# Performance work log

Hardware: AMD Instinct MI355X
Metric: run time of the kernel (lower is better)

## Reference

```python
import jax, jax.numpy as jnp
import numpy as np

N = 50000
E = 800000
H = 96
NUM_IN = 11
PE_DIM = 24
NUM_OUT = 1
NUM_LAYERS = 4
NUM_GRAPHS = 256


def _linear_params(key, d_in, d_out):
    k1, k2 = jax.random.split(key)
    bound = 1.0 / np.sqrt(d_in)
    w = jax.random.uniform(k1, (d_in, d_out), jnp.float32, -bound, bound)
    b = jax.random.uniform(k2, (d_out,), jnp.float32, -bound, bound)
    return w, b


def setup_inputs() -> dict:
    key = jax.random.key(0)
    ks = jax.random.split(key, 32)
    x = jax.random.normal(ks[0], (N, NUM_IN), jnp.float32)
    pos = jax.random.normal(ks[1], (N, 3), jnp.float32)
    pe = jax.random.normal(ks[2], (N, PE_DIM), jnp.float32)
    edge_index = jax.random.randint(ks[3], (2, E), 0, N, jnp.int64)
    batch = jnp.sort(jax.random.randint(ks[4], (N,), 0, NUM_GRAPHS, jnp.int64))
    embed_w1, embed_b1 = _linear_params(ks[5], NUM_IN + PE_DIM, H)
    embed_w2, embed_b2 = _linear_params(ks[6], H, H)
    # per-layer stacked params
    msg_w1 = []; msg_b1 = []; msg_w2 = []; msg_b2 = []
    upd_w1 = []; upd_b1 = []; upd_w2 = []; upd_b2 = []
    for l in range(NUM_LAYERS):
        w, b = _linear_params(ks[7 + l], 2 * H + 1, H); msg_w1.append(w); msg_b1.append(b)
        w, b = _linear_params(ks[11 + l], H, H); msg_w2.append(w); msg_b2.append(b)
        w, b = _linear_params(ks[15 + l], 2 * H, H); upd_w1.append(w); upd_b1.append(b)
        w, b = _linear_params(ks[19 + l], H, H); upd_w2.append(w); upd_b2.append(b)
    pre_w1, pre_b1 = _linear_params(ks[23], H, H)
    pre_w2, pre_b2 = _linear_params(ks[24], H, H)
    ro_w1, ro_b1 = _linear_params(ks[25], H, H)
    ro_w2, ro_b2 = _linear_params(ks[26], H, NUM_OUT)
    return {
        'x': x, 'pos': pos, 'pe': pe, 'edge_index': edge_index, 'batch': batch,
        'embed_w1': embed_w1, 'embed_b1': embed_b1, 'embed_w2': embed_w2, 'embed_b2': embed_b2,
        'msg_w1': jnp.stack(msg_w1), 'msg_b1': jnp.stack(msg_b1),
        'msg_w2': jnp.stack(msg_w2), 'msg_b2': jnp.stack(msg_b2),
        'upd_w1': jnp.stack(upd_w1), 'upd_b1': jnp.stack(upd_b1),
        'upd_w2': jnp.stack(upd_w2), 'upd_b2': jnp.stack(upd_b2),
        'pre_w1': pre_w1, 'pre_b1': pre_b1, 'pre_w2': pre_w2, 'pre_b2': pre_b2,
        'ro_w1': ro_w1, 'ro_b1': ro_b1, 'ro_w2': ro_w2, 'ro_b2': ro_b2,
    }


def _egnn_forward(x, pos, pe, edge_index, batch,
                  embed_w1, embed_b1, embed_w2, embed_b2,
                  msg_w1, msg_b1, msg_w2, msg_b2,
                  upd_w1, upd_b1, upd_w2, upd_b2,
                  pre_w1, pre_b1, pre_w2, pre_b2,
                  ro_w1, ro_b1, ro_w2, ro_b2):
    silu = jax.nn.silu
    send, rec = edge_index[0], edge_index[1]
    h = jnp.concatenate([x, pe], axis=-1)
    h = silu(h @ embed_w1 + embed_b1) @ embed_w2 + embed_b2  # [N,H]
    dist = jnp.linalg.norm(pos[send] - pos[rec], axis=1)[:, None]  # [E,1]
    for l in range(NUM_LAYERS):
        state = jnp.concatenate([h[send], h[rec], dist], axis=1)  # [E,2H+1]
        msg = silu(silu(state @ msg_w1[l] + msg_b1[l]) @ msg_w2[l] + msg_b2[l])  # [E,H]
        aggr = jax.ops.segment_sum(msg, rec, num_segments=h.shape[0])  # [N,H]
        upd_in = jnp.concatenate([h, aggr], axis=1)
        update = silu(upd_in @ upd_w1[l] + upd_b1[l]) @ upd_w2[l] + upd_b2[l]
        h = h + update
    h = silu(h @ pre_w1 + pre_b1) @ pre_w2 + pre_b2
    pooled = jax.ops.segment_sum(h, batch, num_segments=NUM_GRAPHS)  # [G,H]
    out = silu(pooled @ ro_w1 + ro_b1) @ ro_w2 + ro_b2  # [G,1]
    return jnp.squeeze(out)


def reference(x, pos, pe, edge_index, batch,
              embed_w1, embed_b1, embed_w2, embed_b2,
              msg_w1, msg_b1, msg_w2, msg_b2,
              upd_w1, upd_b1, upd_w2, upd_b2,
              pre_w1, pre_b1, pre_w2, pre_b2,
              ro_w1, ro_b1, ro_w2, ro_b2):
    return _egnn_forward(x, pos, pe, edge_index, batch,
                         embed_w1, embed_b1, embed_w2, embed_b2,
                         msg_w1, msg_b1, msg_w2, msg_b2,
                         upd_w1, upd_b1, upd_w2, upd_b2,
                         pre_w1, pre_b1, pre_w2, pre_b2,
                         ro_w1, ro_b1, ro_w2, ro_b2)
```

## Files before the change

### kernel.cpp

```cpp
#include <hip/hip_runtime.h>
#include <hip/hip_bf16.h>

#define HDIM 96
#define TILE 128

typedef __attribute__((ext_vector_type(8))) short  short8;
typedef __attribute__((ext_vector_type(4))) short  short4v;
typedef __attribute__((ext_vector_type(4))) float  float4v;
typedef __attribute__((ext_vector_type(4))) unsigned int uint4v;

static __device__ __forceinline__ short f2bf(float f){
    __hip_bfloat16 h = __float2bfloat16(f);
    return *reinterpret_cast<short*>(&h);
}
static __device__ __forceinline__ float bf2f(short s){
    unsigned u = ((unsigned)(unsigned short)s) << 16;
    return __uint_as_float(u);
}
static __device__ __forceinline__ float silu_f(float v){
    return v * __builtin_amdgcn_rcpf(1.0f + __expf(-v));
}

struct SwJob { const float* src; int ck; int ks; int ksrc; };
struct SwTable { SwJob j[22]; };

__global__ __launch_bounds__(256) void swizzle_kernel(SwTable T, short* __restrict__ dst, int total){
    int gid = blockIdx.x*256 + threadIdx.x;
    if (gid >= total) return;
    int ksg = gid / 3072;
    int e   = gid % 3072;
    const float* src = T.j[0].src; int k0 = 0, ksrc = 0;
    #pragma unroll
    for (int jj = 0; jj < 22; ++jj){
        int s = T.j[jj].ck;
        if (ksg >= s && ksg < s + T.j[jj].ks){ src = T.j[jj].src; k0 = (ksg - s)*32; ksrc = T.j[jj].ksrc; }
    }
    int nt   = e >> 9;
    int rem  = e & 511;
    int lane = rem >> 3;
    int jx   = rem & 7;
    int k = k0 + ((lane >> 4) << 3) + jx;
    int f = nt*16 + (lane & 15);
    float v = (k < ksrc) ? src[(size_t)k*HDIM + f] : 0.0f;
    dst[gid] = f2bf(v);
}

__global__ __launch_bounds__(256) void swizzle2_kernel(const float* __restrict__ msg_w1,
                                                       short* __restrict__ dst, int total){
    int gid = blockIdx.x*256 + threadIdx.x;
    if (gid >= total) return;
    int layer = gid / 18432;
    int e     = gid % 18432;
    int ksg = e / 6144;
    int rem = e % 6144;
    int nt   = rem >> 9;
    int r2   = rem & 511;
    int lane = r2 >> 3;
    int jx   = r2 & 7;
    int k = ksg*32 + ((lane >> 4) << 3) + jx;
    int f = nt*16 + (lane & 15);
    int row = (f < 96) ? k : (96 + k);
    int col = (f < 96) ? f : (f - 96);
    dst[gid] = f2bf(msg_w1[(size_t)layer*193*96 + (size_t)row*96 + col]);
}

__global__ __launch_bounds__(256) void hist_kernel(const int* __restrict__ rec, int* __restrict__ deg, int E){
    int e = blockIdx.x*256 + threadIdx.x;
    if (e < E) atomicAdd(&deg[rec[e]], 1);
}

__global__ __launch_bounds__(256) void scan_part(const int* __restrict__ deg, int* __restrict__ part, int N){
    __shared__ int red[256];
    const int t = threadIdx.x;
    int base = blockIdx.x*1024;
    int s = 0;
    #pragma unroll
    for (int j=0;j<4;j++){ int i = base + j*256 + t; s += (i<N)?deg[i]:0; }
    red[t]=s; __syncthreads();
    #pragma unroll
    for (int off=128; off>0; off>>=1){ if (t<off) red[t]+=red[t+off]; __syncthreads(); }
    if (t==0) part[blockIdx.x]=red[0];
}
__global__ __launch_bounds__(256) void scan_top(int* __restrict__ part, int nb){
    __shared__ int buf[256];
    const int t = threadIdx.x;
    int v = (t < nb) ? part[t] : 0;
    buf[t] = v;
    __syncthreads();
    #pragma unroll
    for (int off=1; off<256; off<<=1){
        int u = (t>=off)?buf[t-off]:0;
        __syncthreads();
        buf[t] += u;
        __syncthreads();
    }
    if (t < nb) part[t] = buf[t] - v;
}
__global__ __launch_bounds__(256) void scan_final(const int* __restrict__ deg, const int* __restrict__ part,
                                                  int* __restrict__ cur, int N){
    __shared__ int tsum[256];
    const int t = threadIdx.x;
    int i0 = blockIdx.x*1024 + t*4;
    int a0 = (i0+0<N)?deg[i0+0]:0;
    int a1 = (i0+1<N)?deg[i0+1]:0;
    int a2 = (i0+2<N)?deg[i0+2]:0;
    int a3 = (i0+3<N)?deg[i0+3]:0;
    int s = a0+a1+a2+a3;
    tsum[t]=s; __syncthreads();
    #pragma unroll
    for (int off=1; off<256; off<<=1){
        int u = (t>=off)?tsum[t-off]:0;
        __syncthreads();
        tsum[t]+=u;
        __syncthreads();
    }
    int excl = tsum[t]-s + part[blockIdx.x];
    if (i0+0<N) cur[i0+0]=excl;
    if (i0+1<N) cur[i0+1]=excl+a0;
    if (i0+2<N) cur[i0+2]=excl+a0+a1;
    if (i0+3<N) cur[i0+3]=excl+a0+a1+a2;
}

__global__ __launch_bounds__(256) void scatter_kernel(
    const int* __restrict__ send, const int* __restrict__ rec, const float* __restrict__ pos,
    int* __restrict__ cur, int* __restrict__ send_s, int* __restrict__ rec_s,
    float* __restrict__ dist_s, int E)
{
    int e = blockIdx.x*256 + threadIdx.x;
    if (e >= E) return;
    int s = send[e], r = rec[e];
    int p = atomicAdd(&cur[r], 1);
    send_s[p] = s;
    rec_s[p]  = r;
    float dx = pos[3*s]   - pos[3*r];
    float dy = pos[3*s+1] - pos[3*r+1];
    float dz = pos[3*s+2] - pos[3*r+2];
    dist_s[p] = sqrtf(dx*dx + dy*dy + dz*dz);
}

__global__ __launch_bounds__(256,5) void edge_kernel(
    const short* __restrict__ SR,
    const int* __restrict__ send_s, const int* __restrict__ rec_s, const float* __restrict__ dist_s,
    const float* __restrict__ w1r192,
    const short* __restrict__ w2sw, const float* __restrict__ b2,
    float* __restrict__ aggr, int E)
{
    __shared__ short msgS[TILE*104];
    __shared__ int   recS[TILE];
    __shared__ int   startIdxS[TILE+1];
    __shared__ int   wcntS[2];
    const int t  = threadIdx.x;
    const int e0 = blockIdx.x * TILE;

    if (t < TILE) {
        int e = e0 + t; if (e >= E) e = E - 1;
        recS[t] = rec_s[e];
    }
    __syncthreads();

    bool flag = false;
    if (t < TILE) flag = (t == 0) || (recS[t] != recS[t-1]);
    unsigned long long bmask = __ballot(flag ? 1 : 0);
    int pre = __popcll(bmask & ((1ull << (t & 63)) - 1ull));
    if (t < TILE && (t & 63) == 0) wcntS[t >> 6] = __popcll(bmask);
    __syncthreads();
    const int nseg = wcntS[0] + wcntS[1];
    if (flag) startIdxS[pre + ((t >> 6) ? wcntS[0] : 0)] = t;
    if (t == 0) startIdxS[nseg] = TILE;

    const bool firstB = (e0 > 0) && (rec_s[e0-1] == recS[0]);
    const bool lastB  = (e0 + TILE < E) && (rec_s[e0 + TILE] == recS[TILE-1]);

    const int lane = t & 63;
    const int wv   = t >> 6;
    const int e_lo = wv * 32;
    const int col  = lane & 15;
    const int quad = lane >> 4;
    const int frow = quad * 4;
    const float4v fzero = {0.f,0.f,0.f,0.f};

    short8 frag[2][3];
    #pragma unroll
    for (int et=0; et<2; ++et){
        int ei = e_lo + et*16 + col;
        int ec = e0 + ei; if (ec >= E) ec = E - 1;
        int se = send_s[ec];
        int re = recS[ei];
        float d = dist_s[ec];
        #pragma unroll
        for (int ks=0; ks<3; ++ks){
            int f0 = ks*32 + quad*8;
            short8 S8 = *(const short8*)(SR + (size_t)se*192 + f0);
            short8 R8 = *(const short8*)(SR + (size_t)re*192 + 96 + f0);
            float4v wa = *(const float4v*)(w1r192 + f0);
            float4v wb = *(const float4v*)(w1r192 + f0 + 4);
            short8 fr;
            #pragma unroll
            for (int j=0;j<8;j++){
                float w = (j<4) ? wa[j] : wb[j-4];
                float v = bf2f(S8[j]) + bf2f(R8[j]) + d*w;
                fr[j] = f2bf(silu_f(v));
            }
            frag[et][ks] = fr;
        }
    }

    float4v acc2[2][6];
    #pragma unroll
    for (int i=0;i<2;i++)
      #pragma unroll
      for (int n=0;n<6;n++) acc2[i][n] = fzero;

    const short8* w2f = (const short8*)w2sw;
    #pragma unroll
    for (int ks = 0; ks < 3; ++ks) {
        #pragma unroll
        for (int mt = 0; mt < 6; ++mt) {
            short8 a = w2f[(ks*6+mt)*64 + lane];
            acc2[0][mt] = __builtin_amdgcn_mfma_f32_16x16x32_bf16(a, frag[0][ks], acc2[0][mt], 0, 0, 0);
            acc2[1][mt] = __builtin_amdgcn_mfma_f32_16x16x32_bf16(a, frag[1][ks], acc2[1][mt], 0, 0, 0);
        }
    }
    float4v b2v[6];
    #pragma unroll
    for (int mt=0; mt<6; ++mt) b2v[mt] = *(const float4v*)(b2 + mt*16 + frow);

    #pragma unroll
    for (int et=0; et<2; ++et){
        int e = e_lo + et*16 + col;
        bool valid = (e0 + e) < E;
        #pragma unroll
        for (int mt=0; mt<6; ++mt){
            short4v sv;
            #pragma unroll
            for (int r=0;r<4;r++){
                float u = silu_f(acc2[et][mt][r] + b2v[mt][r]);
                sv[r] = f2bf(valid ? u : 0.0f);
            }
            *(short4v*)(msgS + e*104 + mt*16 + frow) = sv;
        }
    }
    __syncthreads();

    const int items = nseg * 12;
    for (int item = t; item < items; item += 256){
        int s  = item / 12;
        int fg = item - s*12;
        int r0 = startIdxS[s], r1 = startIdxS[s+1];
        float sum[8] = {0.f,0.f,0.f,0.f,0.f,0.f,0.f,0.f};
        for (int r = r0; r < r1; ++r){
            short8 v8 = *(const short8*)(msgS + r*104 + fg*8);
            #pragma unroll
            for (int j=0;j<8;j++) sum[j] += bf2f(v8[j]);
        }
        float* dstp = aggr + (size_t)recS[r0]*HDIM + fg*8;
        bool bnd = (s == 0 && firstB) || (s == nseg-1 && lastB);
        if (bnd) {
            #pragma unroll
            for (int j=0;j<8;j++) atomicAdd(dstp+j, sum[j]);
        } else {
            float4v lo = {sum[0], sum[1], sum[2], sum[3]};
            float4v hi = {sum[4], sum[5], sum[6], sum[7]};
            *(float4v*)(dstp)     = lo;
            *(float4v*)(dstp + 4) = hi;
        }
    }
}

__global__ __launch_bounds__(256,3) void update_kernel(
    float* __restrict__ h, short* __restrict__ hbf, float* __restrict__ aggr,
    const short* __restrict__ w1sw, const float* __restrict__ b1,
    const short* __restrict__ w2sw, const float* __restrict__ b2,
    const short* __restrict__ w1sr_next, const float* __restrict__ msgb1_next,
    short* __restrict__ SR, int N)
{
    __shared__ short stateS[TILE*200];
    const int t  = threadIdx.x;
    const int n0 = blockIdx.x * TILE;

    #pragma unroll
    for (int it = 0; it < 12; ++it) {
        int q = it*256 + t;
        int c = q % 24;
        int i = q / 24;
        int node = n0 + i;
        if (c < 12) {
            uint4v v = {0u,0u,0u,0u};
            if (node < N) v = *(const uint4v*)(hbf + (size_t)node*HDIM + c*8);
            *(uint4v*)(stateS + i*200 + c*8) = v;
        } else {
            int cc = c - 12;
            short8 s8 = {0,0,0,0,0,0,0,0};
            if (node < N) {
                float4v a0 = *(const float4v*)(aggr + (size_t)node*HDIM + cc*8);
                float4v a1 = *(const float4v*)(aggr + (size_t)node*HDIM + cc*8 + 4);
                s8[0]=f2bf(a0[0]); s8[1]=f2bf(a0[1]); s8[2]=f2bf(a0[2]); s8[3]=f2bf(a0[3]);
                s8[4]=f2bf(a1[0]); s8[5]=f2bf(a1[1]); s8[6]=f2bf(a1[2]); s8[7]=f2bf(a1[3]);
            }
            *(short8*)(stateS + i*200 + HDIM + cc*8) = s8;
        }
    }
    __syncthreads();

    const int lane = t & 63;
    const int wv   = t >> 6;
    const int e_lo = wv * 32;
    const int col  = lane & 15;
    const int quad = lane >> 4;
    const int koff = quad * 8;
    const int frow = quad * 4;
    const float4v fzero = {0.f,0.f,0.f,0.f};

    float4v acc[2][6];
    #pragma unroll
    for (int i=0;i<2;i++)
      #pragma unroll
      for (int n=0;n<6;n++) acc[i][n] = fzero;

    const short8* w1f = (const short8*)w1sw;
    #pragma unroll
    for (int ks = 0; ks < 6; ++ks) {
        short8 bb0 = *(const short8*)(stateS + (e_lo+col)*200    + ks*32 + koff);
        short8 bb1 = *(const short8*)(stateS + (e_lo+16+col)*200 + ks*32 + koff);
        #pragma unroll
        for (int mt = 0; mt < 6; ++mt) {
            short8 a = w1f[(ks*6+mt)*64 + lane];
            acc[0][mt] = __builtin_amdgcn_mfma_f32_16x16x32_bf16(a, bb0, acc[0][mt], 0, 0, 0);
            acc[1][mt] = __builtin_amdgcn_mfma_f32_16x16x32_bf16(a, bb1, acc[1][mt], 0, 0, 0);
        }
    }
    float4v b1v[6];
    #pragma unroll
    for (int mt=0; mt<6; ++mt) b1v[mt] = *(const float4v*)(b1 + mt*16 + frow);
    __syncthreads();

    short* t1S = stateS;
    #pragma unroll
    for (int et=0; et<2; ++et){
        int e = e_lo + et*16 + col;
        #pragma unroll
        for (int mt=0; mt<6; ++mt){
            short4v sv;
            #pragma unroll
            for (int r=0;r<4;r++) sv[r] = f2bf(silu_f(acc[et][mt][r] + b1v[mt][r]));
            *(short4v*)(t1S + e*104 + mt*16 + frow) = sv;
        }
    }
    __syncthreads();

    float4v acc2[2][6];
    #pragma unroll
    for (int i=0;i<2;i++)
      #pragma unroll
      for (int n=0;n<6;n++) acc2[i][n] = fzero;

    const short8* w2f = (const short8*)w2sw;
    #pragma unroll
    for (int ks = 0; ks < 3; ++ks) {
        short8 bb0 = *(const short8*)(t1S + (e_lo+col)*104    + ks*32 + koff);
        short8 bb1 = *(const short8*)(t1S + (e_lo+16+col)*104 + ks*32 + koff);
        #pragma unroll
        for (int mt = 0; mt < 6; ++mt) {
            short8 a = w2f[(ks*6+mt)*64 + lane];
            acc2[0][mt] = __builtin_amdgcn_mfma_f32_16x16x32_bf16(a, bb0, acc2[0][mt], 0, 0, 0);
            acc2[1][mt] = __builtin_amdgcn_mfma_f32_16x16x32_bf16(a, bb1, acc2[1][mt], 0, 0, 0);
        }
    }
    float4v b2v[6];
    #pragma unroll
    for (int mt=0; mt<6; ++mt) b2v[mt] = *(const float4v*)(b2 + mt*16 + frow);
    __syncthreads();

    #pragma unroll
    for (int et=0; et<2; ++et){
        int erow = e_lo + et*16 + col;
        int node = n0 + erow;
        bool valid = node < N;
        size_t base = (size_t)node*HDIM;
        #pragma unroll
        for (int mt=0; mt<6; ++mt){
            int f0 = mt*16 + frow;
            float4v old = valid ? *(const float4v*)(h + base + f0) : fzero;
            float4v o;
            #pragma unroll
            for (int r=0;r<4;r++) o[r] = old[r] + acc2[et][mt][r] + b2v[mt][r];
            short4v sv = {f2bf(o[0]), f2bf(o[1]), f2bf(o[2]), f2bf(o[3])};
            if (valid) {
                *(float4v*)(h + base + f0) = o;
                *(short4v*)(hbf + base + f0) = sv;
                *(float4v*)(aggr + base + f0) = fzero;
            }
            *(short4v*)(stateS + erow*104 + f0) = sv;
        }
    }

    if (w1sr_next) {
        __syncthreads();
        float4v accS[2][12];
        #pragma unroll
        for (int i=0;i<2;i++)
          #pragma unroll
          for (int n=0;n<12;n++) accS[i][n] = fzero;

        const short8* wsf = (const short8*)w1sr_next;
        #pragma unroll
        for (int ks = 0; ks < 3; ++ks) {
            short8 bb0 = *(const short8*)(stateS + (e_lo+col)*104    + ks*32 + koff);
            short8 bb1 = *(const short8*)(stateS + (e_lo+16+col)*104 + ks*32 + koff);
            #pragma unroll
            for (int mt = 0; mt < 12; ++mt) {
                short8 a = wsf[(ks*12+mt)*64 + lane];
                accS[0][mt] = __builtin_amdgcn_mfma_f32_16x16x32_bf16(a, bb0, accS[0][mt], 0, 0, 0);
                accS[1][mt] = __builtin_amdgcn_mfma_f32_16x16x32_bf16(a, bb1, accS[1][mt], 0, 0, 0);
            }
        }
        float4v bnv[6];
        #pragma unroll
        for (int mt=0; mt<6; ++mt) bnv[mt] = *(const float4v*)(msgb1_next + mt*16 + frow);

        #pragma unroll
        for (int et=0; et<2; ++et){
            int node = n0 + e_lo + et*16 + col;
            if (node < N) {
                size_t sbase = (size_t)node*192;
                #pragma unroll
                for (int mt=0; mt<12; ++mt){
                    float4v o = accS[et][mt];
                    if (mt < 6) { o[0]+=bnv[mt][0]; o[1]+=bnv[mt][1]; o[2]+=bnv[mt][2]; o[3]+=bnv[mt][3]; }
                    short4v sv = {f2bf(o[0]), f2bf(o[1]), f2bf(o[2]), f2bf(o[3])};
                    *(short4v*)(SR + sbase + mt*16 + frow) = sv;
                }
            }
        }
    }
}

__global__ __launch_bounds__(256,3) void embed_kernel(
    const float* __restrict__ x, const float* __restrict__ pe,
    const short* __restrict__ w1sw, const float* __restrict__ b1,
    const short* __restrict__ w2sw, const float* __restrict__ b2,
    float* __restrict__ h, short* __restrict__ hbf,
    const short* __restrict__ w1sr0, const float* __restrict__ msgb1_0,
    short* __restrict__ SR, int N)
{
    __shared__ short stateS[TILE*72];
    __shared__ short t1S[TILE*104];
    const int t  = threadIdx.x;
    const int n0 = blockIdx.x * TILE;

    if (t < TILE) {
        int node = n0 + t;
        short* row = stateS + t*72;
        if (node < N) {
            #pragma unroll
            for (int j=0;j<11;j++) row[j]    = f2bf(x[(size_t)node*11 + j]);
            #pragma unroll
            for (int j=0;j<24;j++) row[11+j] = f2bf(pe[(size_t)node*24 + j]);
            #pragma unroll
            for (int j=35;j<64;j++) row[j] = 0;
        } else {
            #pragma unroll
            for (int j=0;j<64;j++) row[j] = 0;
        }
    }
    __syncthreads();

    const int lane = t & 63;
    const int wv   = t >> 6;
    const int e_lo = wv * 32;
    const int col  = lane & 15;
    const int quad = lane >> 4;
    const int koff = quad * 8;
    const int frow = quad * 4;
    const float4v fzero = {0.f,0.f,0.f,0.f};

    float4v acc[2][6];
    #pragma unroll
    for (int i=0;i<2;i++)
      #pragma unroll
      for (int n=0;n<6;n++) acc[i][n] = fzero;

    const short8* w1f = (const short8*)w1sw;
    #pragma unroll
    for (int ks = 0; ks < 2; ++ks) {
        short8 bb0 = *(const short8*)(stateS + (e_lo+col)*72    + ks*32 + koff);
        short8 bb1 = *(const short8*)(stateS + (e_lo+16+col)*72 + ks*32 + koff);
        #pragma unroll
        for (int mt = 0; mt < 6; ++mt) {
            short8 a = w1f[(ks*6+mt)*64 + lane];
            acc[0][mt] = __builtin_amdgcn_mfma_f32_16x16x32_bf16(a, bb0, acc[0][mt], 0, 0, 0);
            acc[1][mt] = __builtin_amdgcn_mfma_f32_16x16x32_bf16(a, bb1, acc[1][mt], 0, 0, 0);
        }
    }
    float4v b1v[6];
    #pragma unroll
    for (int mt=0; mt<6; ++mt) b1v[mt] = *(const float4v*)(b1 + mt*16 + frow);

    #pragma unroll
    for (int et=0; et<2; ++et){
        int e = e_lo + et*16 + col;
        #pragma unroll
        for (int mt=0; mt<6; ++mt){
            short4v sv;
            #pragma unroll
            for (int r=0;r<4;r++) sv[r] = f2bf(silu_f(acc[et][mt][r] + b1v[mt][r]));
            *(short4v*)(t1S + e*104 + mt*16 + frow) = sv;
        }
    }
    __syncthreads();

    float4v acc2[2][6];
    #pragma unroll
    for (int i=0;i<2;i++)
      #pragma unroll
      for (int n=0;n<6;n++) acc2[i][n] = fzero;

    const short8* w2f = (const short8*)w2sw;
    #pragma unroll
    for (int ks = 0; ks < 3; ++ks) {
        short8 bb0 = *(const short8*)(t1S + (e_lo+col)*104    + ks*32 + koff);
        short8 bb1 = *(const short8*)(t1S + (e_lo+16+col)*104 + ks*32 + koff);
        #pragma unroll
        for (int mt = 0; mt < 6; ++mt) {
            short8 a = w2f[(ks*6+mt)*64 + lane];
            acc2[0][mt] = __builtin_amdgcn_mfma_f32_16x16x32_bf16(a, bb0, acc2[0][mt], 0, 0, 0);
            acc2[1][mt] = __builtin_amdgcn_mfma_f32_16x16x32_bf16(a, bb1, acc2[1][mt], 0, 0, 0);
        }
    }
    float4v b2v[6];
    #pragma unroll
    for (int mt=0; mt<6; ++mt) b2v[mt] = *(const float4v*)(b2 + mt*16 + frow);
    __syncthreads();

    #pragma unroll
    for (int et=0; et<2; ++et){
        int erow = e_lo + et*16 + col;
        int node = n0 + erow;
        bool valid = node < N;
        size_t base = (size_t)node*HDIM;
        #pragma unroll
        for (int mt=0; mt<6; ++mt){
            int f0 = mt*16 + frow;
            float4v o;
            #pragma unroll
            for (int r=0;r<4;r++) o[r] = acc2[et][mt][r] + b2v[mt][r];
            short4v sv = {f2bf(o[0]), f2bf(o[1]), f2bf(o[2]), f2bf(o[3])};
            if (valid) {
                *(float4v*)(h + base + f0) = o;
                *(short4v*)(hbf + base + f0) = sv;
            }
            *(short4v*)(t1S + erow*104 + f0) = sv;
        }
    }
    __syncthreads();

    float4v accS[2][12];
    #pragma unroll
    for (int i=0;i<2;i++)
      #pragma unroll
      for (int n=0;n<12;n++) accS[i][n] = fzero;

    const short8* wsf = (const short8*)w1sr0;
    #pragma unroll
    for (int ks = 0; ks < 3; ++ks) {
        short8 bb0 = *(const short8*)(t1S + (e_lo+col)*104    + ks*32 + koff);
        short8 bb1 = *(const short8*)(t1S + (e_lo+16+col)*104 + ks*32 + koff);
        #pragma unroll
        for (int mt = 0; mt < 12; ++mt) {
            short8 a = wsf[(ks*12+mt)*64 + lane];
            accS[0][mt] = __builtin_amdgcn_mfma_f32_16x16x32_bf16(a, bb0, accS[0][mt], 0, 0, 0);
            accS[1][mt] = __builtin_amdgcn_mfma_f32_16x16x32_bf16(a, bb1, accS[1][mt], 0, 0, 0);
        }
    }
    float4v bnv[6];
    #pragma unroll
    for (int mt=0; mt<6; ++mt) bnv[mt] = *(const float4v*)(msgb1_0 + mt*16 + frow);

    #pragma unroll
    for (int et=0; et<2; ++et){
        int node = n0 + e_lo + et*16 + col;
        if (node < N) {
            size_t sbase = (size_t)node*192;
            #pragma unroll
            for (int mt=0; mt<12; ++mt){
                float4v o = accS[et][mt];
                if (mt < 6) { o[0]+=bnv[mt][0]; o[1]+=bnv[mt][1]; o[2]+=bnv[mt][2]; o[3]+=bnv[mt][3]; }
                short4v sv = {f2bf(o[0]), f2bf(o[1]), f2bf(o[2]), f2bf(o[3])};
                *(short4v*)(SR + sbase + mt*16 + frow) = sv;
            }
        }
    }
}

__global__ __launch_bounds__(256,2) void prepool_kernel(
    const short* __restrict__ hbf,
    const short* __restrict__ w1sw, const float* __restrict__ b1,
    const short* __restrict__ w2sw, const float* __restrict__ b2,
    const int* __restrict__ batch, float* __restrict__ pooled, int N)
{
    __shared__ short bufS[TILE*104*2];
    __shared__ int   batchS[TILE];
    __shared__ int   startIdxS[TILE+1];
    __shared__ int   wcntS[2];
    short* stateS = bufS;
    short* t1S    = bufS + TILE*104;
    float* msgS   = (float*)bufS;
    const int t  = threadIdx.x;
    const int n0 = blockIdx.x * TILE;

    #pragma unroll
    for (int it = 0; it < 6; ++it) {
        int q = it*256 + t;
        int c = q % 12;
        int i = q / 12;
        int node = n0 + i;
        uint4v v = {0u,0u,0u,0u};
        if (node < N) v = *(const uint4v*)(hbf + (size_t)node*HDIM + c*8);
        *(uint4v*)(stateS + i*104 + c*8) = v;
    }
    if (t < TILE) {
        int node = n0 + t;
        batchS[t] = batch[node < N ? node : N-1];
    }
    __syncthreads();

    bool flag = false;
    if (t < TILE) flag = (t == 0) || (batchS[t] != batchS[t-1]);
    unsigned long long bmask = __ballot(flag ? 1 : 0);
    int pre = __popcll(bmask & ((1ull << (t & 63)) - 1ull));
    if (t < TILE && (t & 63) == 0) wcntS[t >> 6] = __popcll(bmask);

    const int lane = t & 63;
    const int wv   = t >> 6;
    const int e_lo = wv * 32;
    const int col  = lane & 15;
    const int quad = lane >> 4;
    const int koff = quad * 8;
    const int frow = quad * 4;
    const float4v fzero = {0.f,0.f,0.f,0.f};

    float4v acc[2][6];
    #pragma unroll
    for (int i=0;i<2;i++)
      #pragma unroll
      for (int n=0;n<6;n++) acc[i][n] = fzero;

    const short8* w1f = (const short8*)w1sw;
    #pragma unroll
    for (int ks = 0; ks < 3; ++ks) {
        short8 bb0 = *(const short8*)(stateS + (e_lo+col)*104    + ks*32 + koff);
        short8 bb1 = *(const short8*)(stateS + (e_lo+16+col)*104 + ks*32 + koff);
        #pragma unroll
        for (int mt = 0; mt < 6; ++mt) {
            short8 a = w1f[(ks*6+mt)*64 + lane];
            acc[0][mt] = __builtin_amdgcn_mfma_f32_16x16x32_bf16(a, bb0, acc[0][mt], 0, 0, 0);
            acc[1][mt] = __builtin_amdgcn_mfma_f32_16x16x32_bf16(a, bb1, acc[1][mt], 0, 0, 0);
        }
    }
    float4v b1v[6];
    #pragma unroll
    for (int mt=0; mt<6; ++mt) b1v[mt] = *(const float4v*)(b1 + mt*16 + frow);

    #pragma unroll
    for (int et=0; et<2; ++et){
        int e = e_lo + et*16 + col;
        #pragma unroll
        for (int mt=0; mt<6; ++mt){
            short4v sv;
            #pragma unroll
            for (int r=0;r<4;r++) sv[r] = f2bf(silu_f(acc[et][mt][r] + b1v[mt][r]));
            *(short4v*)(t1S + e*104 + mt*16 + frow) = sv;
        }
    }
    __syncthreads();
    const int nseg = wcntS[0] + wcntS[1];
    if (flag) startIdxS[pre + ((t >> 6) ? wcntS[0] : 0)] = t;
    if (t == 0) startIdxS[nseg] = TILE;

    float4v acc2[2][6];
    #pragma unroll
    for (int i=0;i<2;i++)
      #pragma unroll
      for (int n=0;n<6;n++) acc2[i][n] = fzero;

    const short8* w2f = (const short8*)w2sw;
    #pragma unroll
    for (int ks = 0; ks < 3; ++ks) {
        short8 bb0 = *(const short8*)(t1S + (e_lo+col)*104    + ks*32 + koff);
        short8 bb1 = *(const short8*)(t1S + (e_lo+16+col)*104 + ks*32 + koff);
        #pragma unroll
        for (int mt = 0; mt < 6; ++mt) {
            short8 a = w2f[(ks*6+mt)*64 + lane];
            acc2[0][mt] = __builtin_amdgcn_mfma_f32_16x16x32_bf16(a, bb0, acc2[0][mt], 0, 0, 0);
            acc2[1][mt] = __builtin_amdgcn_mfma_f32_16x16x32_bf16(a, bb1, acc2[1][mt], 0, 0, 0);
        }
    }
    float4v b2v[6];
    #pragma unroll
    for (int mt=0; mt<6; ++mt) b2v[mt] = *(const float4v*)(b2 + mt*16 + frow);
    __syncthreads();

    #pragma unroll
    for (int et=0; et<2; ++et){
        int e = e_lo + et*16 + col;
        bool valid = (n0 + e) < N;
        #pragma unroll
        for (int mt=0; mt<6; ++mt){
            float4v v;
            #pragma unroll
            for (int r=0;r<4;r++){
                float u = acc2[et][mt][r] + b2v[mt][r];
                v[r] = valid ? u : 0.0f;
            }
            *(float4v*)(msgS + e*100 + mt*16 + frow) = v;
        }
    }
    __syncthreads();

    const int items = nseg * 24;
    for (int item = t; item < items; item += 256){
        int s  = item / 24;
        int fg = item - s*24;
        int r0 = startIdxS[s], r1 = startIdxS[s+1];
        float4v sum = fzero;
        for (int r = r0; r < r1; ++r) sum += *(const float4v*)(msgS + r*100 + fg*4);
        float* dstp = pooled + (size_t)batchS[r0]*HDIM + fg*4;
        atomicAdd(dstp+0, sum[0]);
        atomicAdd(dstp+1, sum[1]);
        atomicAdd(dstp+2, sum[2]);
        atomicAdd(dstp+3, sum[3]);
    }
}

__global__ __launch_bounds__(128) void readout_kernel(
    const float* __restrict__ pooled,
    const float* __restrict__ w1, const float* __restrict__ b1,
    const float* __restrict__ w2, const float* __restrict__ b2,
    float* __restrict__ out)
{
    __shared__ float red[128];
    const int g = blockIdx.x;
    const int t = threadIdx.x;
    float p = 0.0f;
    if (t < HDIM) {
        float acc = b1[t];
        for (int k = 0; k < HDIM; ++k)
            acc += pooled[(size_t)g*HDIM + k] * w1[(size_t)k*HDIM + t];
        acc = silu_f(acc);
        p = acc * w2[t];
    }
    red[t] = p;
    __syncthreads();
    for (int s = 64; s > 0; s >>= 1) {
        if (t < s) red[t] += red[t + s];
        __syncthreads();
    }
    if (t == 0) out[g] = red[0] + b2[0];
}

extern "C" void kernel_launch(void* const* d_in, const int* in_sizes, int n_in,
                              void* d_out, int out_size, void* d_ws, size_t ws_size,
                              hipStream_t stream)
{
    const float* x        = (const float*)d_in[0];
    const float* pos      = (const float*)d_in[1];
    const float* pe       = (const float*)d_in[2];
    const int*   ei       = (const int*)d_in[3];
    const int*   batch    = (const int*)d_in[4];
    const float* embed_w1 = (const float*)d_in[5];
    const float* embed_b1 = (const float*)d_in[6];
    const float* embed_w2 = (const float*)d_in[7];
    const float* embed_b2 = (const float*)d_in[8];
    const float* msg_w1   = (const float*)d_in[9];
    const float* msg_b1   = (const float*)d_in[10];
    const float* msg_w2   = (const float*)d_in[11];
    const float* msg_b2   = (const float*)d_in[12];
    const float* upd_w1   = (const float*)d_in[13];
    const float* upd_b1   = (const float*)d_in[14];
    const float* upd_w2   = (const float*)d_in[15];
    const float* upd_b2   = (const float*)d_in[16];
    const float* pre_w1   = (const float*)d_in[17];
    const float* pre_b1   = (const float*)d_in[18];
    const float* pre_w2   = (const float*)d_in[19];
    const float* pre_b2   = (const float*)d_in[20];
    const float* ro_w1    = (const float*)d_in[21];
    const float* ro_b1    = (const float*)d_in[22];
    const float* ro_w2    = (const float*)d_in[23];
    const float* ro_b2    = (const float*)d_in[24];

    const int E = in_sizes[3] / 2;
    const int N = in_sizes[4];
    const int G = out_size;

    char* ws = (char*)d_ws;
    size_t off = 0;
    auto alloc = [&](size_t bytes){ void* p = ws + off; off += (bytes + 255) & ~(size_t)255; return p; };
    float* h      = (float*)alloc((size_t)N*HDIM*4);
    short* hbf    = (short*)alloc((size_t)N*HDIM*2);
    float* aggr   = (float*)alloc((size_t)N*HDIM*4);
    float* pooled = (float*)alloc((size_t)G*HDIM*4);
    short* wsw    = (short*)alloc((size_t)59*3072*2);
    short* w1sr   = (short*)alloc((size_t)4*18432*2);
    short* SR     = (short*)alloc((size_t)N*192*2);
    int*   deg    = (int*)alloc((size_t)N*4);
    int*   cur    = (int*)alloc((size_t)N*4);
    int*   part   = (int*)alloc((size_t)256*4);
    int*   send_s = (int*)alloc((size_t)E*4);
    int*   rec_s  = (int*)alloc((size_t)E*4);
    float* dist_s = (float*)alloc((size_t)E*4);

    hipMemsetAsync(aggr,   0, (size_t)N*HDIM*4, stream);
    hipMemsetAsync(pooled, 0, (size_t)G*HDIM*4, stream);
    hipMemsetAsync(deg,    0, (size_t)N*4, stream);

    SwTable T;
    for (int jj=0;jj<22;jj++){ T.j[jj].src = embed_w1; T.j[jj].ck = 1<<30; T.j[jj].ks = 0; T.j[jj].ksrc = 0; }
    int ck = 0, ji = 0;
    auto add = [&](const float* s, int ks, int ksrc){
        T.j[ji].src = s; T.j[ji].ck = ck; T.j[ji].ks = ks; T.j[ji].ksrc = ksrc;
        ji++; ck += ks;
    };
    add(embed_w1, 2, 35);
    add(embed_w2, 3, 96);
    add(pre_w1,   3, 96);
    add(pre_w2,   3, 96);
    for (int l=0;l<4;l++) add(msg_w2 + (size_t)l*96*96,  3, 96);
    for (int l=0;l<4;l++) add(upd_w1 + (size_t)l*192*96, 6, 192);
    for (int l=0;l<4;l++) add(upd_w2 + (size_t)l*96*96,  3, 96);
    const int total = 59*3072;
    swizzle_kernel<<<(total+255)/256, 256, 0, stream>>>(T, wsw, total);
    const int total2 = 4*18432;
    swizzle2_kernel<<<(total2+255)/256, 256, 0, stream>>>(msg_w1, w1sr, total2);

    const int nbE256 = (E + 255) / 256;
    const int nbScan = (N + 1023) / 1024;
    hist_kernel<<<nbE256, 256, 0, stream>>>(ei + E, deg, E);
    scan_part<<<nbScan, 256, 0, stream>>>(deg, part, N);
    scan_top<<<1, 256, 0, stream>>>(part, nbScan);
    scan_final<<<nbScan, 256, 0, stream>>>(deg, part, cur, N);
    scatter_kernel<<<nbE256, 256, 0, stream>>>(ei, ei + E, pos, cur, send_s, rec_s, dist_s, E);

    const int nbN = (N + TILE - 1) / TILE;
    embed_kernel<<<nbN, 256, 0, stream>>>(x, pe, wsw + 0, embed_b1, wsw + 2*3072, embed_b2,
                                          h, hbf, w1sr, msg_b1, SR, N);

    const int nbE = (E + TILE - 1) / TILE;
    for (int l = 0; l < 4; ++l) {
        edge_kernel<<<nbE, 256, 0, stream>>>(SR, send_s, rec_s, dist_s,
            msg_w1 + (size_t)l*193*96 + (size_t)192*96,
            wsw + (11 + 3*l)*3072, msg_b2 + l*96, aggr, E);
        const short* w1sr_next = (l < 3) ? (w1sr + (size_t)(l+1)*18432) : nullptr;
        const float* msgb1_next = (l < 3) ? (msg_b1 + (l+1)*96) : nullptr;
        update_kernel<<<nbN, 256, 0, stream>>>(h, hbf, aggr,
            wsw + (23 + 6*l)*3072, upd_b1 + l*96,
            wsw + (47 + 3*l)*3072, upd_b2 + l*96,
            w1sr_next, msgb1_next, SR, N);
    }

    prepool_kernel<<<nbN, 256, 0, stream>>>(hbf, wsw + 5*3072, pre_b1, wsw + 8*3072, pre_b2,
                                            batch, pooled, N);
    readout_kernel<<<G, 128, 0, stream>>>(pooled, ro_w1, ro_b1, ro_w2, ro_b2, (float*)d_out);
}
```

Measured before the change: 766.1 us.

## Pack sender/dist into int2, shrink LDS stride, cheaper bf16 round, raise occupancy

Measured after the change: 879.3 us. 1.15x slower.

```diff
diff --git a/kernel.cpp b/kernel.cpp
--- a/kernel.cpp
+++ b/kernel.cpp
@@ -10,8 +10,8 @@
 typedef __attribute__((ext_vector_type(4))) unsigned int uint4v;
 
 static __device__ __forceinline__ short f2bf(float f){
-    __hip_bfloat16 h = __float2bfloat16(f);
-    return *reinterpret_cast<short*>(&h);
+    unsigned u = __float_as_uint(f);
+    return (short)((u + 0x8000u) >> 16);
 }
 static __device__ __forceinline__ float bf2f(short s){
     unsigned u = ((unsigned)(unsigned short)s) << 16;
@@ -123,29 +123,28 @@
 
 __global__ __launch_bounds__(256) void scatter_kernel(
     const int* __restrict__ send, const int* __restrict__ rec, const float* __restrict__ pos,
-    int* __restrict__ cur, int* __restrict__ send_s, int* __restrict__ rec_s,
-    float* __restrict__ dist_s, int E)
+    int* __restrict__ cur, int2* __restrict__ sd_s, int* __restrict__ rec_s, int E)
 {
     int e = blockIdx.x*256 + threadIdx.x;
     if (e >= E) return;
     int s = send[e], r = rec[e];
     int p = atomicAdd(&cur[r], 1);
-    send_s[p] = s;
-    rec_s[p]  = r;
     float dx = pos[3*s]   - pos[3*r];
     float dy = pos[3*s+1] - pos[3*r+1];
     float dz = pos[3*s+2] - pos[3*r+2];
-    dist_s[p] = sqrtf(dx*dx + dy*dy + dz*dz);
-}
-
-__global__ __launch_bounds__(256,5) void edge_kernel(
+    float d = sqrtf(dx*dx + dy*dy + dz*dz);
+    sd_s[p] = make_int2(s, __float_as_int(d));
+    rec_s[p] = r;
+}
+
+__global__ __launch_bounds__(256,6) void edge_kernel(
     const short* __restrict__ SR,
-    const int* __restrict__ send_s, const int* __restrict__ rec_s, const float* __restrict__ dist_s,
+    const int2* __restrict__ sd_s, const int* __restrict__ rec_s,
     const float* __restrict__ w1r192,
     const short* __restrict__ w2sw, const float* __restrict__ b2,
     float* __restrict__ aggr, int E)
 {
-    __shared__ short msgS[TILE*104];
+    __shared__ short msgS[TILE*100];
     __shared__ int   recS[TILE];
     __shared__ int   startIdxS[TILE+1];
     __shared__ int   wcntS[2];
@@ -184,9 +183,10 @@
     for (int et=0; et<2; ++et){
         int ei = e_lo + et*16 + col;
         int ec = e0 + ei; if (ec >= E) ec = E - 1;
-        int se = send_s[ec];
+        int2 sd = sd_s[ec];
+        int se = sd.x;
+        float d = __int_as_float(sd.y);
         int re = recS[ei];
-        float d = dist_s[ec];
         #pragma unroll
         for (int ks=0; ks<3; ++ks){
             int f0 = ks*32 + quad*8;
@@ -237,7 +237,7 @@
                 float u = silu_f(acc2[et][mt][r] + b2v[mt][r]);
                 sv[r] = f2bf(valid ? u : 0.0f);
             }
-            *(short4v*)(msgS + e*104 + mt*16 + frow) = sv;
+            *(short4v*)(msgS + e*100 + mt*16 + frow) = sv;
         }
     }
     __syncthreads();
@@ -249,9 +249,12 @@
         int r0 = startIdxS[s], r1 = startIdxS[s+1];
         float sum[8] = {0.f,0.f,0.f,0.f,0.f,0.f,0.f,0.f};
         for (int r = r0; r < r1; ++r){
-            short8 v8 = *(const short8*)(msgS + r*104 + fg*8);
-            #pragma unroll
-            for (int j=0;j<8;j++) sum[j] += bf2f(v8[j]);
+            short4v a = *(const short4v*)(msgS + r*100 + fg*8);
+            short4v b = *(const short4v*)(msgS + r*100 + fg*8 + 4);
+            #pragma unroll
+            for (int j=0;j<4;j++) sum[j]   += bf2f(a[j]);
+            #pragma unroll
+            for (int j=0;j<4;j++) sum[4+j] += bf2f(b[j]);
         }
         float* dstp = aggr + (size_t)recS[r0]*HDIM + fg*8;
         bool bnd = (s == 0 && firstB) || (s == nseg-1 && lastB);
@@ -805,9 +808,8 @@
     int*   deg    = (int*)alloc((size_t)N*4);
     int*   cur    = (int*)alloc((size_t)N*4);
     int*   part   = (int*)alloc((size_t)256*4);
-    int*   send_s = (int*)alloc((size_t)E*4);
+    int2*  sd_s   = (int2*)alloc((size_t)E*8);
     int*   rec_s  = (int*)alloc((size_t)E*4);
-    float* dist_s = (float*)alloc((size_t)E*4);
 
     hipMemsetAsync(aggr,   0, (size_t)N*HDIM*4, stream);
     hipMemsetAsync(pooled, 0, (size_t)G*HDIM*4, stream);
@@ -838,7 +840,7 @@
     scan_part<<<nbScan, 256, 0, stream>>>(deg, part, N);
     scan_top<<<1, 256, 0, stream>>>(part, nbScan);
     scan_final<<<nbScan, 256, 0, stream>>>(deg, part, cur, N);
-    scatter_kernel<<<nbE256, 256, 0, stream>>>(ei, ei + E, pos, cur, send_s, rec_s, dist_s, E);
+    scatter_kernel<<<nbE256, 256, 0, stream>>>(ei, ei + E, pos, cur, sd_s, rec_s, E);
 
     const int nbN = (N + TILE - 1) / TILE;
     embed_kernel<<<nbN, 256, 0, stream>>>(x, pe, wsw + 0, embed_b1, wsw + 2*3072, embed_b2,
@@ -846,7 +848,7 @@
 
     const int nbE = (E + TILE - 1) / TILE;
     for (int l = 0; l < 4; ++l) {
-        edge_kernel<<<nbE, 256, 0, stream>>>(SR, send_s, rec_s, dist_s,
+        edge_kernel<<<nbE, 256, 0, stream>>>(SR, sd_s, rec_s,
             msg_w1 + (size_t)l*193*96 + (size_t)192*96,
             wsw + (11 + 3*l)*3072, msg_b2 + l*96, aggr, E);
         const short* w1sr_next = (l < 3) ? (w1sr + (size_t)(l+1)*18432) : nullptr;
```
